# Kernel tuning notes

Hardware: AMD Instinct MI355X
Metric: run time of the kernel (lower is better)

Reference implementation:

```python
import jax, jax.numpy as jnp
import numpy as np

N_NODES = 50000
N_EDGES = 400000
F_IN = 128
F_EDGE = 32
F_HID = 32
N_HEADS = 4
N_LAYERS = 2


def _edge_softmax(alpha_raw, dst, num_nodes):
    # alpha_raw: (E, H). The original flattens (E,H,1) edge-major with segment id
    # dst[e] for EVERY head, so normalization runs over all incoming edges AND all
    # heads of a node (heads share one softmax). dim_size N*H in the original only
    # adds never-read empty segments, so N segments is numerically identical.
    node_max = jax.ops.segment_max(jnp.max(alpha_raw, axis=1), dst, num_segments=num_nodes)
    exp_a = jnp.exp(alpha_raw - node_max[dst][:, None])
    node_sum = jax.ops.segment_sum(jnp.sum(exp_a, axis=1), dst, num_segments=num_nodes)
    return exp_a / (node_sum[dst][:, None] + 1e-8)


def _layer(h, edge_attr, src, dst, p):
    # h: (N, H, F); edge_attr: (E, Fe); src=edge_index[0], dst=edge_index[1]
    (asw, asb, adw, adb, aew, aeb, dw, db, mdw, mdb, mew, meb, wnw, wnb) = p
    N, H, F = h.shape
    E = src.shape[0]
    xs = h @ asw + asb                       # attn_src(x): (N,H,F)
    xd = h @ adw + adb                       # attn_dst(x): (N,H,F)
    ea = edge_attr @ aew + aeb               # attn_edg(e): (E,F)
    attn_in = jax.nn.relu(xs[dst] + xd[src] + ea[:, None, :])   # (E,H,F)
    alpha_raw = (attn_in @ dw + db)[..., 0]                     # attn_dot: (E,H)
    alpha = _edge_softmax(alpha_raw, dst, N)                    # (E,H)
    xm = h @ mdw + mdb                       # msg_dst(x): (N,H,F)
    em = edge_attr @ mew + meb               # msg_edg(e): (E,F)
    msg = (alpha[..., None] * (xm[dst] + em[:, None, :])).reshape(E * H, F)
    # Original: edge_index.repeat(1, H) (head-tiled) paired with edge-major
    # (e,h)-flattened messages -> message k=e*H+h is scattered to dst[k mod E].
    idx = jnp.tile(dst, H)                   # (E*H,)
    aggr = jax.ops.segment_sum(msg, idx, num_segments=N * H).reshape(N, H, F)
    return aggr + (h @ wnw + wnb)            # + wgt_n(x)


def _forward(x, edge_attr, edge_index, atom_w, atom_b, layer_params):
    src, dst = edge_index[0], edge_index[1]
    N = x.shape[0]
    atom_in = jax.nn.relu((x @ atom_w + atom_b).reshape(N, N_HEADS, F_HID))
    h = atom_in
    for l in range(N_LAYERS):
        p = tuple(w[l] for w in layer_params)
        h = jax.nn.relu(_layer(h, edge_attr, src, dst, p) + atom_in)
    return h.mean(axis=1)                    # (N, F_HID)


def setup_inputs() -> dict:
    key = jax.random.key(0)
    ks = jax.random.split(key, 20)
    s = 0.05
    rn = lambda k, sh: jax.random.normal(k, sh, dtype=jnp.float32)
    L, F, Fe = N_LAYERS, F_HID, F_EDGE
    z = lambda sh: jnp.zeros(sh, jnp.float32)
    return {
        "x": rn(ks[0], (N_NODES, F_IN)),
        "edge_attr": rn(ks[1], (N_EDGES, Fe)),
        "edge_index": jax.random.randint(ks[2], (2, N_EDGES), 0, N_NODES, dtype=jnp.int32),
        "atom_w": rn(ks[3], (F_IN, F * N_HEADS)) * s,
        "atom_b": z((F * N_HEADS,)),
        "attn_src_w": rn(ks[4], (L, F, F)) * s, "attn_src_b": z((L, F)),
        "attn_dst_w": rn(ks[5], (L, F, F)) * s, "attn_dst_b": z((L, F)),
        "attn_edg_w": rn(ks[6], (L, Fe, F)) * s, "attn_edg_b": z((L, F)),
        "attn_dot_w": rn(ks[7], (L, F, 1)) * s, "attn_dot_b": z((L, 1)),
        "msg_dst_w": rn(ks[8], (L, F, F)) * s, "msg_dst_b": z((L, F)),
        "msg_edg_w": rn(ks[9], (L, Fe, F)) * s, "msg_edg_b": z((L, F)),
        "wgt_n_w": rn(ks[10], (L, F, F)) * s, "wgt_n_b": z((L, F)),
    }


def reference(x, edge_attr, edge_index, atom_w, atom_b, attn_src_w, attn_src_b,
              attn_dst_w, attn_dst_b, attn_edg_w, attn_edg_b, attn_dot_w, attn_dot_b,
              msg_dst_w, msg_dst_b, msg_edg_w, msg_edg_b, wgt_n_w, wgt_n_b):
    lp = (attn_src_w, attn_src_b, attn_dst_w, attn_dst_b, attn_edg_w, attn_edg_b,
          attn_dot_w, attn_dot_b, msg_dst_w, msg_dst_b, msg_edg_w, msg_edg_b,
          wgt_n_w, wgt_n_b)
    return _forward(x, edge_attr, edge_index, atom_w, atom_b, lp)
```

## Files before the change

kernel.cpp:

```cpp
#include <hip/hip_runtime.h>

#define N_NODES 50000
#define N_EDGES 400000
#define EQ      100000
#define F_IN    128
#define F_EDGE  32
#define F       32
#define H       4
#define NHF     128

#define SCAN_BLK 512
#define N_SCAN_BLKS ((N_NODES + SCAN_BLK - 1) / SCAN_BLK)

__device__ __forceinline__ float bf2f(unsigned short u) {
    return __uint_as_float(((unsigned)u) << 16);
}
__device__ __forceinline__ unsigned short f2bf(float f) {
    unsigned u = __float_as_uint(f);
    return (unsigned short)((u + 0x7FFFu + ((u >> 16) & 1u)) >> 16);
}
__device__ __forceinline__ ushort4 pack4(float4 v) {
    return make_ushort4(f2bf(v.x), f2bf(v.y), f2bf(v.z), f2bf(v.w));
}

__global__ __launch_bounds__(256) void k_atom(const float* __restrict__ x,
                                              const float* __restrict__ w,
                                              const float* __restrict__ b,
                                              float* __restrict__ out) {
    __shared__ float wlds[F_IN * NHF];
    __shared__ float xl[32 * F_IN];
    const float4* w4 = (const float4*)w;
    float4* wl4 = (float4*)wlds;
    for (int i = threadIdx.x; i < F_IN * NHF / 4; i += 256) wl4[i] = w4[i];
    int nb = blockIdx.x * 32;
    int nrows = min(32, N_NODES - nb);
    const float4* x4 = (const float4*)(x + (size_t)nb * F_IN);
    float4* xl4 = (float4*)xl;
    for (int i = threadIdx.x; i < nrows * F_IN / 4; i += 256) xl4[i] = x4[i];
    __syncthreads();
    int jg = threadIdx.x & 31;
    int nl = threadIdx.x >> 5;
    float4 bv = *(const float4*)(b + jg * 4);
    float4 acc[4] = {bv, bv, bv, bv};
    for (int k = 0; k < F_IN; k++) {
        float4 wv = *(const float4*)(wlds + k * NHF + jg * 4);
#pragma unroll
        for (int q = 0; q < 4; q++) {
            float xk = xl[(nl + 8 * q) * F_IN + k];
            acc[q].x += xk * wv.x; acc[q].y += xk * wv.y;
            acc[q].z += xk * wv.z; acc[q].w += xk * wv.w;
        }
    }
#pragma unroll
    for (int q = 0; q < 4; q++) {
        int n = nb + nl + 8 * q;
        if (n < N_NODES) {
            float4 a = acc[q];
            a.x = fmaxf(a.x, 0.f); a.y = fmaxf(a.y, 0.f);
            a.z = fmaxf(a.z, 0.f); a.w = fmaxf(a.w, 0.f);
            *(float4*)(out + (size_t)n * NHF + jg * 4) = a;
        }
    }
}

__global__ __launch_bounds__(256) void k_hist(const int* __restrict__ dst,
                                              int* __restrict__ counts) {
    int e = blockIdx.x * 256 + threadIdx.x;
    if (e < N_EDGES) atomicAdd(counts + dst[e], 1);
}

__global__ __launch_bounds__(SCAN_BLK) void k_scan1(const int* __restrict__ counts,
        int* __restrict__ excl, int* __restrict__ bsum) {
    __shared__ int s[SCAN_BLK];
    int i = blockIdx.x * SCAN_BLK + threadIdx.x;
    int v = (i < N_NODES) ? counts[i] : 0;
    s[threadIdx.x] = v;
    __syncthreads();
    for (int d = 1; d < SCAN_BLK; d <<= 1) {
        int t = (threadIdx.x >= d) ? s[threadIdx.x - d] : 0;
        __syncthreads();
        s[threadIdx.x] += t;
        __syncthreads();
    }
    if (i < N_NODES) excl[i] = s[threadIdx.x] - v;
    if (threadIdx.x == SCAN_BLK - 1) bsum[blockIdx.x] = s[SCAN_BLK - 1];
}

__global__ __launch_bounds__(128) void k_scan2(int* __restrict__ bsum) {
    __shared__ int s[128];
    int v = (threadIdx.x < N_SCAN_BLKS) ? bsum[threadIdx.x] : 0;
    s[threadIdx.x] = v;
    __syncthreads();
    for (int d = 1; d < 128; d <<= 1) {
        int t = (threadIdx.x >= d) ? s[threadIdx.x - d] : 0;
        __syncthreads();
        s[threadIdx.x] += t;
        __syncthreads();
    }
    if (threadIdx.x < N_SCAN_BLKS) bsum[threadIdx.x] = s[threadIdx.x] - v;
}

__global__ __launch_bounds__(SCAN_BLK) void k_scan3(const int* __restrict__ excl,
        const int* __restrict__ bsum, int* __restrict__ row_start,
        int* __restrict__ cursor) {
    int i = blockIdx.x * SCAN_BLK + threadIdx.x;
    if (i < N_NODES) {
        int v = excl[i] + bsum[blockIdx.x];
        row_start[i] = v;
        cursor[i] = v;
    }
}

__global__ __launch_bounds__(256) void k_fill(const int* __restrict__ src,
        const int* __restrict__ dst, int* __restrict__ cursor,
        int* __restrict__ csr_e, int* __restrict__ srcp,
        int* __restrict__ inv_pos) {
    int e = blockIdx.x * 256 + threadIdx.x;
    if (e < N_EDGES) {
        int pos = atomicAdd(cursor + dst[e], 1);
        csr_e[pos] = e;
        srcp[pos] = src[e];
        inv_pos[e] = pos;
    }
}

__global__ __launch_bounds__(256) void k_nodelin3(const float* __restrict__ h,
        const float* __restrict__ ws, const float* __restrict__ bs,
        const float* __restrict__ wd, const float* __restrict__ bd,
        const float* __restrict__ wm, const float* __restrict__ bm,
        unsigned short* __restrict__ xs, unsigned short* __restrict__ xd,
        unsigned short* __restrict__ xm) {
    __shared__ float Ws[F * F], Wd[F * F], Wm[F * F];
    __shared__ float hrt[F][64];
    for (int i = threadIdx.x; i < F * F; i += 256) {
        Ws[i] = ws[i]; Wd[i] = wd[i]; Wm[i] = wm[i];
    }
    int rbase = blockIdx.x * 64;
    for (int i = threadIdx.x; i < 512; i += 256) {
        int row = i >> 3, kq = i & 7;
        float4 v = *(const float4*)(h + (size_t)(rbase + row) * F + kq * 4);
        hrt[kq * 4 + 0][row] = v.x; hrt[kq * 4 + 1][row] = v.y;
        hrt[kq * 4 + 2][row] = v.z; hrt[kq * 4 + 3][row] = v.w;
    }
    __syncthreads();
    int rl = threadIdx.x >> 2;
    int jg = threadIdx.x & 3;
    float4 s0 = *(const float4*)(bs + jg * 8), s1 = *(const float4*)(bs + jg * 8 + 4);
    float4 d0 = *(const float4*)(bd + jg * 8), d1 = *(const float4*)(bd + jg * 8 + 4);
    float4 m0 = *(const float4*)(bm + jg * 8), m1 = *(const float4*)(bm + jg * 8 + 4);
    for (int k = 0; k < F; k++) {
        float hv = hrt[k][rl];
        float4 a, b2;
        a = *(const float4*)(Ws + k * F + jg * 8); b2 = *(const float4*)(Ws + k * F + jg * 8 + 4);
        s0.x += hv * a.x; s0.y += hv * a.y; s0.z += hv * a.z; s0.w += hv * a.w;
        s1.x += hv * b2.x; s1.y += hv * b2.y; s1.z += hv * b2.z; s1.w += hv * b2.w;
        a = *(const float4*)(Wd + k * F + jg * 8); b2 = *(const float4*)(Wd + k * F + jg * 8 + 4);
        d0.x += hv * a.x; d0.y += hv * a.y; d0.z += hv * a.z; d0.w += hv * a.w;
        d1.x += hv * b2.x; d1.y += hv * b2.y; d1.z += hv * b2.z; d1.w += hv * b2.w;
        a = *(const float4*)(Wm + k * F + jg * 8); b2 = *(const float4*)(Wm + k * F + jg * 8 + 4);
        m0.x += hv * a.x; m0.y += hv * a.y; m0.z += hv * a.z; m0.w += hv * a.w;
        m1.x += hv * b2.x; m1.y += hv * b2.y; m1.z += hv * b2.z; m1.w += hv * b2.w;
    }
    size_t o = (size_t)(rbase + rl) * F + jg * 8;
    *(ushort4*)(xs + o) = pack4(s0); *(ushort4*)(xs + o + 4) = pack4(s1);
    *(ushort4*)(xd + o) = pack4(d0); *(ushort4*)(xd + o + 4) = pack4(d1);
    *(ushort4*)(xm + o) = pack4(m0); *(ushort4*)(xm + o + 4) = pack4(m1);
}

__global__ __launch_bounds__(256) void k_edgepair(const float* __restrict__ edge_attr,
        const float* __restrict__ aew, const float* __restrict__ aeb,
        const float* __restrict__ mew, const float* __restrict__ meb,
        const int* __restrict__ inv_pos, unsigned short* __restrict__ ea_csr,
        unsigned short* __restrict__ emX) {
    __shared__ float Wa[F_EDGE * F], Wm2[F_EDGE * F];
    __shared__ float ert[F_EDGE][64];
    for (int i = threadIdx.x; i < F_EDGE * F; i += 256) {
        Wa[i] = aew[i]; Wm2[i] = mew[i];
    }
    int ebase = blockIdx.x * 64;
    for (int i = threadIdx.x; i < 512; i += 256) {
        int row = i >> 3, kq = i & 7;
        float4 v = *(const float4*)(edge_attr + (size_t)(ebase + row) * F_EDGE + kq * 4);
        ert[kq * 4 + 0][row] = v.x; ert[kq * 4 + 1][row] = v.y;
        ert[kq * 4 + 2][row] = v.z; ert[kq * 4 + 3][row] = v.w;
    }
    __syncthreads();
    int el = threadIdx.x >> 2;
    int jg = threadIdx.x & 3;
    float4 a0 = *(const float4*)(aeb + jg * 8), a1 = *(const float4*)(aeb + jg * 8 + 4);
    float4 m0 = *(const float4*)(meb + jg * 8), m1 = *(const float4*)(meb + jg * 8 + 4);
    for (int k = 0; k < F_EDGE; k++) {
        float ev = ert[k][el];
        float4 w0, w1;
        w0 = *(const float4*)(Wa + k * F + jg * 8); w1 = *(const float4*)(Wa + k * F + jg * 8 + 4);
        a0.x += ev * w0.x; a0.y += ev * w0.y; a0.z += ev * w0.z; a0.w += ev * w0.w;
        a1.x += ev * w1.x; a1.y += ev * w1.y; a1.z += ev * w1.z; a1.w += ev * w1.w;
        w0 = *(const float4*)(Wm2 + k * F + jg * 8); w1 = *(const float4*)(Wm2 + k * F + jg * 8 + 4);
        m0.x += ev * w0.x; m0.y += ev * w0.y; m0.z += ev * w0.z; m0.w += ev * w0.w;
        m1.x += ev * w1.x; m1.y += ev * w1.y; m1.z += ev * w1.z; m1.w += ev * w1.w;
    }
    int e = ebase + el;
    int p = inv_pos[e];
    size_t oa = (size_t)p * F + jg * 8;
    *(ushort4*)(ea_csr + oa) = pack4(a0);
    *(ushort4*)(ea_csr + oa + 4) = pack4(a1);
    int q = e % EQ, j = e / EQ;
    size_t om = (size_t)q * NHF + j * F + jg * 8;
    *(ushort4*)(emX + om) = pack4(m0);
    *(ushort4*)(emX + om + 4) = pack4(m1);
}

__global__ __launch_bounds__(256) void k_attn(const unsigned short* __restrict__ ea_csr,
        const unsigned short* __restrict__ xs, const unsigned short* __restrict__ xd,
        const int* __restrict__ srcp, const int* __restrict__ row_start,
        const int* __restrict__ counts, const int* __restrict__ csr_e,
        const float* __restrict__ dw, const float* __restrict__ db,
        float* __restrict__ alphaT) {
    __shared__ float lg[4][512];
    int wv = threadIdx.x >> 6, lane = threadIdx.x & 63;
    int n = blockIdx.x * 4 + wv;
    if (n >= N_NODES) return;
    int start = row_start[n];
    int items = counts[n] * 4;
    float4 wreg[8];
#pragma unroll
    for (int q = 0; q < 8; q++) wreg[q] = *(const float4*)(dw + q * 4);
    float dbv = db[0];
    const unsigned short* xsr = xs + (size_t)n * NHF;
    float m = -1e30f;
    for (int i = lane; i < items; i += 64) {
        int ii = i >> 2, hh = i & 3;
        int p = start + ii;
        int s = srcp[p];
        const unsigned short* ear = ea_csr + (size_t)p * F;
        const unsigned short* xsh = xsr + hh * F;
        const unsigned short* xdh = xd + (size_t)s * NHF + hh * F;
        float acc = 0.f;
#pragma unroll
        for (int q = 0; q < 8; q++) {
            ushort4 ue = *(const ushort4*)(ear + q * 4);
            ushort4 ua = *(const ushort4*)(xsh + q * 4);
            ushort4 ub = *(const ushort4*)(xdh + q * 4);
            acc += fmaxf(bf2f(ua.x) + bf2f(ub.x) + bf2f(ue.x), 0.f) * wreg[q].x;
            acc += fmaxf(bf2f(ua.y) + bf2f(ub.y) + bf2f(ue.y), 0.f) * wreg[q].y;
            acc += fmaxf(bf2f(ua.z) + bf2f(ub.z) + bf2f(ue.z), 0.f) * wreg[q].z;
            acc += fmaxf(bf2f(ua.w) + bf2f(ub.w) + bf2f(ue.w), 0.f) * wreg[q].w;
        }
        float l = acc + dbv;
        lg[wv][i] = l;
        m = fmaxf(m, l);
    }
#pragma unroll
    for (int d = 1; d < 64; d <<= 1) m = fmaxf(m, __shfl_xor(m, d));
    float ssum = 0.f;
    for (int i = lane; i < items; i += 64) ssum += __expf(lg[wv][i] - m);
#pragma unroll
    for (int d = 1; d < 64; d <<= 1) ssum += __shfl_xor(ssum, d);
    float inv = 1.f / (ssum + 1e-8f);
    for (int i = lane; i < items; i += 64) {
        int ii = i >> 2, hh = i & 3;
        int e = csr_e[start + ii];
        float a = __expf(lg[wv][i] - m) * inv;
        alphaT[(size_t)(e % EQ) * 16 + hh * 4 + (e / EQ)] = a;
    }
}

__global__ __launch_bounds__(256) void k_msgq(const float* __restrict__ alphaT,
        const unsigned short* __restrict__ emX, const unsigned short* __restrict__ xm,
        const int* __restrict__ dst, const int* __restrict__ inv_pos,
        unsigned short* __restrict__ ems_csr) {
    int g = blockIdx.x * 8 + (threadIdx.x >> 5);
    if (g >= EQ) return;
    int f = threadIdx.x & 31;
    const float4* a4 = (const float4*)(alphaT + (size_t)g * 16);
    float4 ac[4] = {a4[0], a4[1], a4[2], a4[3]};
    int4 dj = make_int4(dst[g], dst[g + EQ], dst[g + 2 * EQ], dst[g + 3 * EQ]);
    float out[4] = {0.f, 0.f, 0.f, 0.f};
#pragma unroll
    for (int j = 0; j < 4; j++) {
        int d = (j == 0) ? dj.x : (j == 1) ? dj.y : (j == 2) ? dj.z : dj.w;
        float emv = bf2f(emX[(size_t)g * NHF + j * F + f]);
        const unsigned short* xr = xm + (size_t)d * NHF + f;
#pragma unroll
        for (int c = 0; c < 4; c++) {
            float a = (j == 0) ? ac[c].x : (j == 1) ? ac[c].y
                    : (j == 2) ? ac[c].z : ac[c].w;
            out[c] += a * (bf2f(xr[c * F]) + emv);
        }
    }
    const int4 pos = *(const int4*)(inv_pos + (size_t)g * 4);
#pragma unroll
    for (int c = 0; c < 4; c++) {
        int p = (c == 0) ? pos.x : (c == 1) ? pos.y : (c == 2) ? pos.z : pos.w;
        ems_csr[(size_t)p * F + f] = f2bf(out[c]);
    }
}

__global__ __launch_bounds__(128) void k_combine(const float* __restrict__ h,
        const unsigned short* __restrict__ ems_csr, const int* __restrict__ row_start,
        const int* __restrict__ counts, const float* __restrict__ atom_in,
        const float* __restrict__ wn, const float* __restrict__ bn,
        float* __restrict__ hout, float* __restrict__ final_out, int is_final) {
    __shared__ float W[F * F];
    __shared__ float sm[NHF];
    for (int i = threadIdx.x; i < F * F; i += 128) W[i] = wn[i];
    __syncthreads();
    int n = blockIdx.x;
    int head = threadIdx.x >> 5, j = threadIdx.x & 31;
    const float* hr = h + (size_t)n * NHF + head * F;
    float acc = bn[j];
    for (int k = 0; k < F; k++) acc += hr[k] * W[k * F + j];
    float ag = 0.f;
    int m = n * H + head;
    if (m < N_NODES) {
        int st = row_start[m], deg = counts[m];
        const unsigned short* er = ems_csr + (size_t)st * F + j;
        for (int p = 0; p < deg; p++) ag += bf2f(er[(size_t)p * F]);
    }
    size_t idx = (size_t)n * NHF + head * F + j;
    float v = ag + acc + atom_in[idx];
    v = fmaxf(v, 0.f);
    if (!is_final) {
        hout[idx] = v;
    } else {
        sm[threadIdx.x] = v;
        __syncthreads();
        if (threadIdx.x < F) {
            float o = 0.25f * (sm[threadIdx.x] + sm[F + threadIdx.x] +
                               sm[2 * F + threadIdx.x] + sm[3 * F + threadIdx.x]);
            final_out[(size_t)n * F + threadIdx.x] = o;
        }
    }
}

extern "C" void kernel_launch(void* const* d_in, const int* in_sizes, int n_in,
                              void* d_out, int out_size, void* d_ws, size_t ws_size,
                              hipStream_t stream) {
    const float* x         = (const float*)d_in[0];
    const float* edge_attr = (const float*)d_in[1];
    const int*   eidx      = (const int*)d_in[2];
    const int*   src       = eidx;
    const int*   dst       = eidx + N_EDGES;
    const float* atom_w    = (const float*)d_in[3];
    const float* atom_b    = (const float*)d_in[4];
    const float* asw = (const float*)d_in[5],  *asb = (const float*)d_in[6];
    const float* adw = (const float*)d_in[7],  *adb = (const float*)d_in[8];
    const float* aew = (const float*)d_in[9],  *aeb = (const float*)d_in[10];
    const float* dww = (const float*)d_in[11], *dwb = (const float*)d_in[12];
    const float* mdw = (const float*)d_in[13], *mdb = (const float*)d_in[14];
    const float* mew = (const float*)d_in[15], *meb = (const float*)d_in[16];
    const float* wnw = (const float*)d_in[17], *wnb = (const float*)d_in[18];
    float* out = (float*)d_out;

    float* ws = (float*)d_ws;
    size_t off = 0;
    float* atom_in = ws + off; off += (size_t)N_NODES * NHF;
    float* hbuf    = ws + off; off += (size_t)N_NODES * NHF;
    unsigned short* xs_bf  = (unsigned short*)(ws + off); off += (size_t)N_NODES * NHF / 2;
    unsigned short* xd_bf  = (unsigned short*)(ws + off); off += (size_t)N_NODES * NHF / 2;
    unsigned short* xm_bf  = (unsigned short*)(ws + off); off += (size_t)N_NODES * NHF / 2;
    unsigned short* ea_csr = (unsigned short*)(ws + off); off += (size_t)N_EDGES * F / 2;
    unsigned short* emX    = (unsigned short*)(ws + off); off += (size_t)N_EDGES * F / 2;
    unsigned short* ems    = (unsigned short*)(ws + off); off += (size_t)N_EDGES * F / 2;
    float* alphaT  = ws + off; off += (size_t)N_EDGES * H;
    int* counts    = (int*)(ws + off); off += N_NODES;
    int* row_start = (int*)(ws + off); off += N_NODES;
    int* cursor    = (int*)(ws + off); off += N_NODES;
    int* excl      = (int*)(ws + off); off += N_NODES;
    int* bsum      = (int*)(ws + off); off += 128;
    int* csr_e     = (int*)(ws + off); off += N_EDGES;
    int* srcp      = (int*)(ws + off); off += N_EDGES;
    int* inv_pos   = (int*)(ws + off); off += N_EDGES;

    hipMemsetAsync(counts, 0, N_NODES * sizeof(int), stream);
    k_hist <<<(N_EDGES + 255) / 256, 256, 0, stream>>>(dst, counts);
    k_scan1<<<N_SCAN_BLKS, SCAN_BLK, 0, stream>>>(counts, excl, bsum);
    k_scan2<<<1, 128, 0, stream>>>(bsum);
    k_scan3<<<N_SCAN_BLKS, SCAN_BLK, 0, stream>>>(excl, bsum, row_start, cursor);
    k_fill <<<(N_EDGES + 255) / 256, 256, 0, stream>>>(src, dst, cursor, csr_e,
                                                       srcp, inv_pos);

    k_atom<<<(N_NODES + 31) / 32, 256, 0, stream>>>(x, atom_w, atom_b, atom_in);

    for (int l = 0; l < 2; l++) {
        const float* hin  = (l == 0) ? atom_in : hbuf;
        float*       hout = hbuf;
        int is_final = (l == 1);
        k_nodelin3<<<(N_NODES * H) / 64, 256, 0, stream>>>(
            hin, asw + l * F * F, asb + l * F, adw + l * F * F, adb + l * F,
            mdw + l * F * F, mdb + l * F, xs_bf, xd_bf, xm_bf);
        k_edgepair<<<N_EDGES / 64, 256, 0, stream>>>(
            edge_attr, aew + l * F_EDGE * F, aeb + l * F,
            mew + l * F_EDGE * F, meb + l * F, inv_pos, ea_csr, emX);
        k_attn<<<(N_NODES + 3) / 4, 256, 0, stream>>>(
            ea_csr, xs_bf, xd_bf, srcp, row_start, counts, csr_e,
            dww + l * F, dwb + l, alphaT);
        k_msgq<<<(EQ + 7) / 8, 256, 0, stream>>>(alphaT, emX, xm_bf, dst,
                                                 inv_pos, ems);
        k_combine<<<N_NODES, 128, 0, stream>>>(hin, ems, row_start, counts,
                                               atom_in, wnw + l * F * F,
                                               wnb + l * F, hout, out, is_final);
    }
}
```

Measured before the change: 633.5 us.

## Tile combine kernel over 64 head-rows per block with vectorized loads

```diff
diff --git a/kernel.cpp b/kernel.cpp
--- a/kernel.cpp
+++ b/kernel.cpp
@@ -296,39 +296,83 @@
     }
 }
 
-__global__ __launch_bounds__(128) void k_combine(const float* __restrict__ h,
+__global__ __launch_bounds__(256) void k_combine(const float* __restrict__ h,
         const unsigned short* __restrict__ ems_csr, const int* __restrict__ row_start,
         const int* __restrict__ counts, const float* __restrict__ atom_in,
         const float* __restrict__ wn, const float* __restrict__ bn,
         float* __restrict__ hout, float* __restrict__ final_out, int is_final) {
     __shared__ float W[F * F];
-    __shared__ float sm[NHF];
-    for (int i = threadIdx.x; i < F * F; i += 128) W[i] = wn[i];
-    __syncthreads();
-    int n = blockIdx.x;
-    int head = threadIdx.x >> 5, j = threadIdx.x & 31;
-    const float* hr = h + (size_t)n * NHF + head * F;
-    float acc = bn[j];
-    for (int k = 0; k < F; k++) acc += hr[k] * W[k * F + j];
-    float ag = 0.f;
-    int m = n * H + head;
+    __shared__ float hrt[F][64];
+    __shared__ float smv[64][F + 4];
+    for (int i = threadIdx.x; i < F * F; i += 256) W[i] = wn[i];
+    int rbase = blockIdx.x * 64;
+    for (int i = threadIdx.x; i < 512; i += 256) {
+        int row = i >> 3, kq = i & 7;
+        float4 v = *(const float4*)(h + (size_t)(rbase + row) * F + kq * 4);
+        hrt[kq * 4 + 0][row] = v.x; hrt[kq * 4 + 1][row] = v.y;
+        hrt[kq * 4 + 2][row] = v.z; hrt[kq * 4 + 3][row] = v.w;
+    }
+    __syncthreads();
+    int rl = threadIdx.x >> 2;
+    int jg = threadIdx.x & 3;
+    float4 a0 = *(const float4*)(bn + jg * 8);
+    float4 a1 = *(const float4*)(bn + jg * 8 + 4);
+    for (int k = 0; k < F; k++) {
+        float hv = hrt[k][rl];
+        float4 w0 = *(const float4*)(W + k * F + jg * 8);
+        float4 w1 = *(const float4*)(W + k * F + jg * 8 + 4);
+        a0.x += hv * w0.x; a0.y += hv * w0.y; a0.z += hv * w0.z; a0.w += hv * w0.w;
+        a1.x += hv * w1.x; a1.y += hv * w1.y; a1.z += hv * w1.z; a1.w += hv * w1.w;
+    }
+    int m = rbase + rl;
+    float4 g0 = make_float4(0.f, 0.f, 0.f, 0.f);
+    float4 g1 = make_float4(0.f, 0.f, 0.f, 0.f);
     if (m < N_NODES) {
         int st = row_start[m], deg = counts[m];
-        const unsigned short* er = ems_csr + (size_t)st * F + j;
-        for (int p = 0; p < deg; p++) ag += bf2f(er[(size_t)p * F]);
-    }
-    size_t idx = (size_t)n * NHF + head * F + j;
-    float v = ag + acc + atom_in[idx];
-    v = fmaxf(v, 0.f);
+        const unsigned short* er = ems_csr + (size_t)st * F + jg * 8;
+        int p = 0;
+        for (; p + 2 <= deg; p += 2) {
+            ushort4 u0 = *(const ushort4*)(er);
+            ushort4 u1 = *(const ushort4*)(er + 4);
+            ushort4 v0 = *(const ushort4*)(er + F);
+            ushort4 v1 = *(const ushort4*)(er + F + 4);
+            g0.x += bf2f(u0.x) + bf2f(v0.x); g0.y += bf2f(u0.y) + bf2f(v0.y);
+            g0.z += bf2f(u0.z) + bf2f(v0.z); g0.w += bf2f(u0.w) + bf2f(v0.w);
+            g1.x += bf2f(u1.x) + bf2f(v1.x); g1.y += bf2f(u1.y) + bf2f(v1.y);
+            g1.z += bf2f(u1.z) + bf2f(v1.z); g1.w += bf2f(u1.w) + bf2f(v1.w);
+            er += 2 * F;
+        }
+        if (p < deg) {
+            ushort4 u0 = *(const ushort4*)(er);
+            ushort4 u1 = *(const ushort4*)(er + 4);
+            g0.x += bf2f(u0.x); g0.y += bf2f(u0.y);
+            g0.z += bf2f(u0.z); g0.w += bf2f(u0.w);
+            g1.x += bf2f(u1.x); g1.y += bf2f(u1.y);
+            g1.z += bf2f(u1.z); g1.w += bf2f(u1.w);
+        }
+    }
+    size_t idx = (size_t)m * F + jg * 8;
+    float4 t0 = *(const float4*)(atom_in + idx);
+    float4 t1 = *(const float4*)(atom_in + idx + 4);
+    float4 v0, v1;
+    v0.x = fmaxf(a0.x + g0.x + t0.x, 0.f); v0.y = fmaxf(a0.y + g0.y + t0.y, 0.f);
+    v0.z = fmaxf(a0.z + g0.z + t0.z, 0.f); v0.w = fmaxf(a0.w + g0.w + t0.w, 0.f);
+    v1.x = fmaxf(a1.x + g1.x + t1.x, 0.f); v1.y = fmaxf(a1.y + g1.y + t1.y, 0.f);
+    v1.z = fmaxf(a1.z + g1.z + t1.z, 0.f); v1.w = fmaxf(a1.w + g1.w + t1.w, 0.f);
     if (!is_final) {
-        hout[idx] = v;
+        *(float4*)(hout + idx) = v0;
+        *(float4*)(hout + idx + 4) = v1;
     } else {
-        sm[threadIdx.x] = v;
+        *(float4*)(&smv[rl][jg * 8]) = v0;
+        *(float4*)(&smv[rl][jg * 8 + 4]) = v1;
         __syncthreads();
-        if (threadIdx.x < F) {
-            float o = 0.25f * (sm[threadIdx.x] + sm[F + threadIdx.x] +
-                               sm[2 * F + threadIdx.x] + sm[3 * F + threadIdx.x]);
-            final_out[(size_t)n * F + threadIdx.x] = o;
+#pragma unroll
+        for (int it = 0; it < 2; it++) {
+            int oi = threadIdx.x + it * 256;
+            int nl = oi >> 5, f = oi & 31;
+            float o = 0.25f * (smv[nl * 4 + 0][f] + smv[nl * 4 + 1][f] +
+                               smv[nl * 4 + 2][f] + smv[nl * 4 + 3][f]);
+            final_out[((size_t)(rbase >> 2) + nl) * F + f] = o;
         }
     }
 }
@@ -397,8 +441,8 @@
             dww + l * F, dwb + l, alphaT);
         k_msgq<<<(EQ + 7) / 8, 256, 0, stream>>>(alphaT, emX, xm_bf, dst,
                                                  inv_pos, ems);
-        k_combine<<<N_NODES, 128, 0, stream>>>(hin, ems, row_start, counts,
-                                               atom_in, wnw + l * F * F,
-                                               wnb + l * F, hout, out, is_final);
-    }
-}
+        k_combine<<<(N_NODES * H) / 64, 256, 0, stream>>>(
+            hin, ems, row_start, counts, atom_in, wnw + l * F * F,
+            wnb + l * F, hout, out, is_final);
+    }
+}
```

New measurement: 583.4 us. 7.9% less time.
